# Kernel optimization log

Measured on AMD Instinct MI355X. Metric: run time of the kernel, lower is better.

Reference implementation:

```python
import jax, jax.numpy as jnp
import numpy as np

DIM = 1024
HEADS = 16
DIM_HEAD = 64
INNER = HEADS * DIM_HEAD
SCALE = DIM_HEAD ** -0.5
CAUSAL = True


def setup_inputs() -> dict:
    key = jax.random.key(0)
    k1, k2, k3, k4 = jax.random.split(key, 4)
    b, n = 4, 2048
    x = jax.random.normal(k1, (b, n, DIM), dtype=jnp.float32)
    mask = jnp.ones((b, n), dtype=bool)
    w_qkv = jax.random.normal(k2, (DIM, 3 * INNER), dtype=jnp.float32) * (DIM ** -0.5)
    w_out = jax.random.normal(k3, (INNER, DIM), dtype=jnp.float32) * (INNER ** -0.5)
    ln_g = jnp.ones((DIM,), dtype=jnp.float32)
    return {"x": x, "mask": mask, "w_qkv": w_qkv, "w_out": w_out, "ln_g": ln_g}


def clip_layernorm(x, g):
    eps = 1e-5 if x.dtype == jnp.float32 else 1e-3
    mean = jnp.mean(x, axis=-1, keepdims=True)
    var = jnp.var(x, axis=-1, keepdims=True)  # unbiased=False
    return (x - mean) * jax.lax.rsqrt(var + eps) * g


def reference(x, mask, w_qkv, w_out, ln_g):
    b, n, _ = x.shape
    qkv = x @ w_qkv  # [b, n, 3*inner]
    q, k, v = jnp.split(qkv, 3, axis=-1)
    split_heads = lambda t: t.reshape(b, n, HEADS, DIM_HEAD).transpose(0, 2, 1, 3)
    q, k, v = split_heads(q), split_heads(k), split_heads(v)
    q = q * SCALE
    sim = jnp.einsum('bhid,bhjd->bhij', q, k)
    mask_value = -jnp.finfo(sim.dtype).max
    sim = jnp.where(mask[:, None, None, :], sim, mask_value)
    if CAUSAL:
        causal_mask = jnp.triu(jnp.ones((n, n), dtype=bool), k=1)
        sim = jnp.where(causal_mask, mask_value, sim)
    attn = jax.nn.softmax(sim.astype(jnp.float32), axis=-1).astype(sim.dtype)
    out = jnp.einsum('bhij,bhjd->bhid', attn, v)
    out = out.transpose(0, 2, 1, 3).reshape(b, n, INNER)
    out = out @ w_out
    return clip_layernorm(out, ln_g)
```

## Files before the change

### kernel.cpp

```cpp
#include <hip/hip_runtime.h>


typedef unsigned short u16;
typedef __attribute__((ext_vector_type(8))) short bf16x8;
typedef __attribute__((ext_vector_type(4))) float f32x4;
typedef __attribute__((ext_vector_type(4))) unsigned short u16x4;
typedef __attribute__((ext_vector_type(2))) unsigned u32x2;

#define B_SZ  4
#define NSEQ  2048
#define DIMM  1024
#define NQKV  3072
#define MROWS 8192

#define AS_GLOBAL __attribute__((address_space(1)))
#define AS_LDS    __attribute__((address_space(3)))

__device__ __forceinline__ void async_copy16(void* lds, const void* g) {
  __builtin_amdgcn_global_load_lds((const AS_GLOBAL void*)g, (AS_LDS void*)lds, 16, 0, 0);
}

__device__ __forceinline__ u16 f32_to_bf16(float f) {
  unsigned u = __float_as_uint(f);
  u += 0x7FFFu + ((u >> 16) & 1u);
  return (u16)(u >> 16);
}

__device__ __forceinline__ unsigned cvt_pk_bf16(float a, float b) {
  unsigned r;
  asm("v_cvt_pk_bf16_f32 %0, %1, %2" : "=v"(r) : "v"(a), "v"(b));
  return r;
}


__global__ __launch_bounds__(256) void cvt_bf16_k(const float* __restrict__ in,
                                                  u16* __restrict__ out, int n4) {
  int i = blockIdx.x * 256 + threadIdx.x;
  if (i >= n4) return;
  f32x4 v = ((const f32x4*)in)[i];
  u16x4 o;
  #pragma unroll
  for (int c = 0; c < 4; ++c) o[c] = f32_to_bf16(v[c]);
  ((u16x4*)out)[i] = o;
}

__global__ __launch_bounds__(256) void tconv_k(const float* __restrict__ in,
                                               u16* __restrict__ out, int K, int N) {
  __shared__ float tile[64][65];
  int n0 = blockIdx.x * 64, k0 = blockIdx.y * 64;
  int t = threadIdx.x, tr = t >> 6, tc = t & 63;
  #pragma unroll
  for (int i = 0; i < 16; ++i)
    tile[tr + i * 4][tc] = in[(size_t)(k0 + tr + i * 4) * N + n0 + tc];
  __syncthreads();
  #pragma unroll
  for (int i = 0; i < 16; ++i)
    out[(size_t)(n0 + tr + i * 4) * K + k0 + tc] = f32_to_bf16(tile[tc][tr + i * 4]);
}


template<int WN>
__device__ __forceinline__ void gemm_mainloop(const u16* __restrict__ A, const u16* __restrict__ Bt,
                                              int K, size_t arow0, size_t brow0,
                                              u16* lA, u16* lB, f32x4 acc[8][4]) {
  constexpr int NW   = 2 * WN;
  constexpr int BN   = WN * 64;
  constexpr int ASZ  = 256 * 64;
  constexpr int BSZ  = BN * 64;
  constexpr int AIPW = 32 / NW;
  constexpr int BIPW = (BN / 8) / NW;
  const int t = threadIdx.x;
  const int w = t >> 6, lane = t & 63;
  const int l4 = lane >> 4, l15 = lane & 15;
  const int wrow = w / WN, wcol = w % WN;
  const int lr = lane >> 3, lc = lane & 7;

  auto stage = [&](int kt, int bufi) {
    u16* dA = lA + bufi * ASZ;
    u16* dB = lB + bufi * BSZ;
    #pragma unroll
    for (int j = 0; j < AIPW; ++j) {
      int r = w * (256 / NW) + j * 8 + lr;
      async_copy16(&dA[(size_t)r * 64 + lc * 8],
                   &A[(arow0 + r) * (size_t)K + kt + (lc ^ lr) * 8]);
    }
    #pragma unroll
    for (int j = 0; j < BIPW; ++j) {
      int r = w * (BN / NW) + j * 8 + lr;
      async_copy16(&dB[(size_t)r * 64 + lc * 8],
                   &Bt[(brow0 + r) * (size_t)K + kt + (lc ^ lr) * 8]);
    }
  };

  auto phase = [&](int bufi, int ch, bool do_stage, int kt_next, int bufn, bool gate) {
    const u16* bA = lA + bufi * ASZ;
    const u16* bB = lB + bufi * BSZ;
    bf16x8 af[8], bf[4];
    #pragma unroll
    for (int m = 0; m < 8; ++m) {
      int row = wrow * 128 + m * 16 + l15;
      af[m] = *(const bf16x8*)&bA[(size_t)row * 64 + ((ch * 4 + l4) ^ (row & 7)) * 8];
    }
    #pragma unroll
    for (int n = 0; n < 4; ++n) {
      int row = wcol * 64 + n * 16 + l15;
      bf[n] = *(const bf16x8*)&bB[(size_t)row * 64 + ((ch * 4 + l4) ^ (row & 7)) * 8];
    }
    if (do_stage) stage(kt_next, bufn);
    __builtin_amdgcn_s_barrier();
    asm volatile("s_waitcnt lgkmcnt(0)" ::: "memory");
    __builtin_amdgcn_sched_barrier(0);
    __builtin_amdgcn_s_setprio(1);
    #pragma unroll
    for (int m = 0; m < 8; ++m)
      #pragma unroll
      for (int n = 0; n < 4; ++n)
        acc[m][n] = __builtin_amdgcn_mfma_f32_16x16x32_bf16(af[m], bf[n], acc[m][n], 0, 0, 0);
    __builtin_amdgcn_s_setprio(0);
    if (gate) asm volatile("s_waitcnt vmcnt(0)" ::: "memory");
    __builtin_amdgcn_s_barrier();
  };

  const int T = K >> 6;
  stage(0, 0);
  asm volatile("s_waitcnt vmcnt(0)" ::: "memory");
  __builtin_amdgcn_s_barrier();
  #pragma unroll 1
  for (int s = 0; s < T; ++s) {
    const bool st = (s + 1 < T);
    phase(s & 1, 0, st, (s + 1) * 64, (s + 1) & 1, false);
    phase(s & 1, 1, false, 0, 0, st);
  }
}

__global__ __launch_bounds__(512, 2) void gemm_qkv_k(const u16* __restrict__ A, const u16* __restrict__ Bt,
                                                     u16* __restrict__ qb, u16* __restrict__ kb,
                                                     u16* __restrict__ vtb) {
  __shared__ u16 lA[2 * 256 * 64];
  __shared__ u16 lB[2 * 256 * 64];
  f32x4 acc[8][4];
  #pragma unroll
  for (int m = 0; m < 8; ++m)
    #pragma unroll
    for (int n = 0; n < 4; ++n) acc[m][n] = (f32x4){0.f, 0.f, 0.f, 0.f};
  gemm_mainloop<4>(A, Bt, DIMM, (size_t)blockIdx.y * 256, (size_t)blockIdx.x * 256, lA, lB, acc);
  const int t = threadIdx.x, w = t >> 6, lane = t & 63;
  const int l4 = lane >> 4, l15 = lane & 15;
  const int wrow = w >> 2, wcol = w & 3;
  const float QSCALE = 0.125f * 1.44269504089f;
  #pragma unroll
  for (int m = 0; m < 8; ++m)
    #pragma unroll
    for (int n = 0; n < 4; ++n)
      #pragma unroll
      for (int r = 0; r < 4; ++r) {
        int row = blockIdx.y * 256 + wrow * 128 + m * 16 + l4 * 4 + r;
        int col = blockIdx.x * 256 + wcol * 64 + n * 16 + l15;
        float v = acc[m][n][r];
        int bb = row >> 11, nr = row & 2047;
        int part = col >> 10, rem = col & 1023;
        int h = rem >> 6, d = rem & 63;
        int bh = bb * 16 + h;
        if (part == 0)      qb[((size_t)bh * NSEQ + nr) * 64 + d] = f32_to_bf16(v * QSCALE);
        else if (part == 1) kb[((size_t)bh * NSEQ + nr) * 64 + d] = f32_to_bf16(v);
        else                vtb[((size_t)bh * 64 + d) * NSEQ + nr] = f32_to_bf16(v);
      }
}

__global__ __launch_bounds__(256, 1) void gemm_out_k(const u16* __restrict__ A, const u16* __restrict__ Bt,
                                                     float* __restrict__ C) {
  __shared__ u16 lA[2 * 256 * 64];
  __shared__ u16 lB[2 * 128 * 64];
  f32x4 acc[8][4];
  #pragma unroll
  for (int m = 0; m < 8; ++m)
    #pragma unroll
    for (int n = 0; n < 4; ++n) acc[m][n] = (f32x4){0.f, 0.f, 0.f, 0.f};
  gemm_mainloop<2>(A, Bt, DIMM, (size_t)blockIdx.y * 256, (size_t)blockIdx.x * 128, lA, lB, acc);
  const int t = threadIdx.x, w = t >> 6, lane = t & 63;
  const int l4 = lane >> 4, l15 = lane & 15;
  const int wrow = w >> 1, wcol = w & 1;
  #pragma unroll
  for (int m = 0; m < 8; ++m)
    #pragma unroll
    for (int n = 0; n < 4; ++n)
      #pragma unroll
      for (int r = 0; r < 4; ++r) {
        int row = blockIdx.y * 256 + wrow * 128 + m * 16 + l4 * 4 + r;
        int col = blockIdx.x * 128 + wcol * 64 + n * 16 + l15;
        C[(size_t)row * DIMM + col] = acc[m][n][r];
      }
}


__global__ __launch_bounds__(512, 4) void attn_k(const u16* __restrict__ qb, const u16* __restrict__ kb,
                                                 const u16* __restrict__ vtb, u16* __restrict__ ao) {
  __shared__ u16 lK[2][64 * 64];
  __shared__ u16 lV[2][64 * 64];
  __shared__ u16 lP[8][16 * 64];
  const int bh = blockIdx.y;
  const int t = threadIdx.x, w = t >> 6, l = t & 63;
  const int l4 = l >> 4, l15 = l & 15;
  const int b = bh >> 4, h = bh & 15;
  u16* lPw = lP[w];

  const int srow = t >> 3;
  const int ssc = (t & 7) ^ (srow & 7);

  #pragma unroll 1
  for (int phase = 0; phase < 2; ++phase) {
    const int qt = phase == 0 ? (int)blockIdx.x : 15 - (int)blockIdx.x;
    const int q0w = qt * 128 + w * 16;

    bf16x8 qf0 = *(const bf16x8*)&qb[((size_t)bh * NSEQ + q0w + l15) * 64 + l4 * 8];
    bf16x8 qf1 = *(const bf16x8*)&qb[((size_t)bh * NSEQ + q0w + l15) * 64 + 32 + l4 * 8];

    float m_r = -1e30f, l_r = 0.f;
    f32x4 o[4];
    #pragma unroll
    for (int d = 0; d < 4; ++d) o[d] = (f32x4){0.f, 0.f, 0.f, 0.f};

    const int njt = 2 * qt + 2;

    {
      async_copy16(&lK[0][t * 8], &kb[((size_t)bh * NSEQ + srow) * 64 + ssc * 8]);
      async_copy16(&lV[0][t * 8], &vtb[((size_t)bh * 64 + srow) * NSEQ + ssc * 8]);
    }
    int buf = 0;

    for (int jt = 0; jt < njt; ++jt) {
      __syncthreads();
      if (jt + 1 < njt) {
        int bsel = buf ^ 1, jn = jt + 1;
        async_copy16(&lK[bsel][t * 8], &kb[((size_t)bh * NSEQ + jn * 64 + srow) * 64 + ssc * 8]);
        async_copy16(&lV[bsel][t * 8], &vtb[((size_t)bh * 64 + srow) * NSEQ + (size_t)jn * 64 + ssc * 8]);
      }
      const int jt64 = jt * 64;
      if (jt64 > q0w + 15) { buf ^= 1; continue; }
      const u16* Kb = lK[buf];
      const u16* Vb = lV[buf];

      bf16x8 kf[4][2];
      #pragma unroll
      for (int nf = 0; nf < 4; ++nf)
        #pragma unroll
        for (int kk = 0; kk < 2; ++kk)
          kf[nf][kk] = *(const bf16x8*)&Kb[(nf * 16 + l15) * 64 + ((kk * 4 + l4) ^ (l15 & 7)) * 8];

      f32x4 z[4];
      __builtin_amdgcn_s_setprio(1);
      #pragma unroll
      for (int nf = 0; nf < 4; ++nf) {
        f32x4 zz = (f32x4){0.f, 0.f, 0.f, 0.f};
        zz = __builtin_amdgcn_mfma_f32_16x16x32_bf16(kf[nf][0], qf0, zz, 0, 0, 0);
        zz = __builtin_amdgcn_mfma_f32_16x16x32_bf16(kf[nf][1], qf1, zz, 0, 0, 0);
        z[nf] = zz;
      }
      __builtin_amdgcn_s_setprio(0);

      bf16x8 bv[4][2];
      #pragma unroll
      for (int dd = 0; dd < 4; ++dd)
        #pragma unroll
        for (int kk = 0; kk < 2; ++kk)
          bv[dd][kk] = *(const bf16x8*)&Vb[(dd * 16 + l15) * 64 + ((kk * 4 + l4) ^ (l15 & 7)) * 8];

      if (jt64 + 63 > q0w) {
        #pragma unroll
        for (int nf = 0; nf < 4; ++nf)
          #pragma unroll
          for (int r = 0; r < 4; ++r)
            if (jt64 + nf * 16 + l4 * 4 + r > q0w + l15) z[nf][r] = -1e30f;
      }

      float mt = fmaxf(fmaxf(z[0][0], z[0][1]), fmaxf(z[0][2], z[0][3]));
      #pragma unroll
      for (int nf = 1; nf < 4; ++nf)
        mt = fmaxf(mt, fmaxf(fmaxf(z[nf][0], z[nf][1]), fmaxf(z[nf][2], z[nf][3])));
      mt = fmaxf(mt, __shfl_xor(mt, 16));
      mt = fmaxf(mt, __shfl_xor(mt, 32));

      if (!__all(mt <= m_r + 8.f)) {
        float nm = fmaxf(m_r, mt);
        float sc = __builtin_amdgcn_exp2f(m_r - nm);
        m_r = nm;
        l_r *= sc;
        float scr[4];
        #pragma unroll
        for (int r = 0; r < 4; ++r) scr[r] = __shfl(sc, l4 * 4 + r);
        #pragma unroll
        for (int d = 0; d < 4; ++d)
          #pragma unroll
          for (int r = 0; r < 4; ++r) o[d][r] *= scr[r];
      }

      float rs = 0.f;
      unsigned pk[4][2];
      #pragma unroll
      for (int nf = 0; nf < 4; ++nf)
        #pragma unroll
        for (int hh = 0; hh < 2; ++hh) {
          float p0 = __builtin_amdgcn_exp2f(z[nf][2 * hh]     - m_r);
          float p1 = __builtin_amdgcn_exp2f(z[nf][2 * hh + 1] - m_r);
          rs += p0 + p1;
          pk[nf][hh] = cvt_pk_bf16(p0, p1);
        }
      rs += __shfl_xor(rs, 16);
      rs += __shfl_xor(rs, 32);
      l_r += rs;

      #pragma unroll
      for (int nf = 0; nf < 4; ++nf) {
        int u = (2 * nf + (l4 >> 1)) ^ (l15 & 7);
        *(u32x2*)&lPw[l15 * 64 + u * 8 + (l4 & 1) * 4] = (u32x2){pk[nf][0], pk[nf][1]};
      }
      __builtin_amdgcn_sched_barrier(0);
      int u0 = l4 ^ (l15 & 7), u1 = (4 + l4) ^ (l15 & 7);
      bf16x8 af0 = *(const bf16x8*)&lPw[l15 * 64 + u0 * 8];
      bf16x8 af1 = *(const bf16x8*)&lPw[l15 * 64 + u1 * 8];

      __builtin_amdgcn_s_setprio(1);
      #pragma unroll
      for (int d = 0; d < 4; ++d) {
        o[d] = __builtin_amdgcn_mfma_f32_16x16x32_bf16(af0, bv[d][0], o[d], 0, 0, 0);
        o[d] = __builtin_amdgcn_mfma_f32_16x16x32_bf16(af1, bv[d][1], o[d], 0, 0, 0);
      }
      __builtin_amdgcn_s_setprio(0);
      buf ^= 1;
    }

    float lv[4];
    #pragma unroll
    for (int r = 0; r < 4; ++r) lv[r] = __shfl(l_r, l4 * 4 + r);
    #pragma unroll
    for (int d = 0; d < 4; ++d)
      #pragma unroll
      for (int r = 0; r < 4; ++r) {
        int nrow = q0w + l4 * 4 + r;
        float vv = o[d][r] / lv[r];
        ao[((size_t)(b * NSEQ + nrow)) * 1024 + h * 64 + d * 16 + l15] = f32_to_bf16(vv);
      }
  }
}

__global__ __launch_bounds__(256) void ln_k(float* __restrict__ io, const float* __restrict__ g) {
  const int row = blockIdx.x, t = threadIdx.x;
  const int w = t >> 6, l = t & 63;
  f32x4 v = ((const f32x4*)(io + (size_t)row * DIMM))[t];
  float s = v[0] + v[1] + v[2] + v[3];
  float q = v[0] * v[0] + v[1] * v[1] + v[2] * v[2] + v[3] * v[3];
  #pragma unroll
  for (int off = 1; off < 64; off <<= 1) { s += __shfl_xor(s, off); q += __shfl_xor(q, off); }
  __shared__ float ss[8];
  if (l == 0) { ss[w] = s; ss[4 + w] = q; }
  __syncthreads();
  s = ss[0] + ss[1] + ss[2] + ss[3];
  q = ss[4] + ss[5] + ss[6] + ss[7];
  float mean = s * (1.f / DIMM);
  float var = q * (1.f / DIMM) - mean * mean;
  float rstd = rsqrtf(var + 1e-5f);
  f32x4 gv = ((const f32x4*)g)[t];
  f32x4 y;
  #pragma unroll
  for (int c = 0; c < 4; ++c) y[c] = (v[c] - mean) * rstd * gv[c];
  ((f32x4*)(io + (size_t)row * DIMM))[t] = y;
}

extern "C" void kernel_launch(void* const* d_in, const int* in_sizes, int n_in,
                              void* d_out, int out_size, void* d_ws, size_t ws_size,
                              hipStream_t stream) {
  const float* x     = (const float*)d_in[0];
  const float* w_qkv = (const float*)d_in[2];
  const float* w_out = (const float*)d_in[3];
  const float* ln_g  = (const float*)d_in[4];
  float* out = (float*)d_out;

  char* ws = (char*)d_ws;
  const size_t MB = 1u << 20;
  u16* x_bf   = (u16*)(ws);
  u16* wqkv_t = (u16*)(ws + 16 * MB);
  u16* wout_t = (u16*)(ws + 22 * MB);
  u16* qb     = (u16*)(ws + 24 * MB);
  u16* kb     = (u16*)(ws + 40 * MB);
  u16* vtb    = (u16*)(ws + 56 * MB);
  u16* attn_o = x_bf;

  cvt_bf16_k<<<8192, 256, 0, stream>>>(x, x_bf, (MROWS * DIMM) / 4);
  tconv_k<<<dim3(NQKV / 64, DIMM / 64), 256, 0, stream>>>(w_qkv, wqkv_t, DIMM, NQKV);
  tconv_k<<<dim3(DIMM / 64, DIMM / 64), 256, 0, stream>>>(w_out, wout_t, DIMM, DIMM);
  gemm_qkv_k<<<dim3(NQKV / 256, MROWS / 256), 512, 0, stream>>>(x_bf, wqkv_t, qb, kb, vtb);
  attn_k<<<dim3(8, B_SZ * 16), 512, 0, stream>>>(qb, kb, vtb, attn_o);
  gemm_out_k<<<dim3(DIMM / 128, MROWS / 256), 256, 0, stream>>>(attn_o, wout_t, out);
  ln_k<<<MROWS, 256, 0, stream>>>(out, ln_g);
}
```

Baseline: 227.2 us.

## Restructure GEMM mainloop into four-phase split staging and shrink out-proj tiles

Replaces the two-phase GEMM mainloop with a four-quadrant schedule. A and B tiles are staged in halves interleaved between MFMA groups, and partial vmcnt waits let global-to-LDS copies overlap compute at finer granularity. The output projection GEMM moves from 256x128 to 128x128 tiles with two blocks per CU, doubling the grid for better occupancy and load balance. The risk is extra barrier and LDS-read overhead, plus the correctness of the partial vmcnt accounting.

```diff
diff --git a/kernel.cpp b/kernel.cpp
--- a/kernel.cpp
+++ b/kernel.cpp
@@ -59,77 +59,126 @@
 }
 
 
-template<int WN>
-__device__ __forceinline__ void gemm_mainloop(const u16* __restrict__ A, const u16* __restrict__ Bt,
-                                              int K, size_t arow0, size_t brow0,
-                                              u16* lA, u16* lB, f32x4 acc[8][4]) {
-  constexpr int NW   = 2 * WN;
-  constexpr int BN   = WN * 64;
-  constexpr int ASZ  = 256 * 64;
-  constexpr int BSZ  = BN * 64;
-  constexpr int AIPW = 32 / NW;
-  constexpr int BIPW = (BN / 8) / NW;
+template<int BM, int BN, int NW, int MR>
+__device__ __forceinline__ void gemm_loop(const u16* __restrict__ A, const u16* __restrict__ Bt,
+                                          int K, size_t arow0, size_t brow0,
+                                          u16* lA, u16* lB, f32x4 (&acc)[MR][4]) {
+  constexpr int WN  = BN / 64;
+  constexpr int MH  = MR / 2;
+  constexpr int WTM = 16 * MR;
+  constexpr int ASZ = BM * 64;
+  constexpr int BSZ = BN * 64;
   const int t = threadIdx.x;
   const int w = t >> 6, lane = t & 63;
   const int l4 = lane >> 4, l15 = lane & 15;
   const int wrow = w / WN, wcol = w % WN;
   const int lr = lane >> 3, lc = lane & 7;
 
-  auto stage = [&](int kt, int bufi) {
-    u16* dA = lA + bufi * ASZ;
-    u16* dB = lB + bufi * BSZ;
-    #pragma unroll
-    for (int j = 0; j < AIPW; ++j) {
-      int r = w * (256 / NW) + j * 8 + lr;
-      async_copy16(&dA[(size_t)r * 64 + lc * 8],
-                   &A[(arow0 + r) * (size_t)K + kt + (lc ^ lr) * 8]);
-    }
-    #pragma unroll
-    for (int j = 0; j < BIPW; ++j) {
-      int r = w * (BN / NW) + j * 8 + lr;
-      async_copy16(&dB[(size_t)r * 64 + lc * 8],
-                   &Bt[(brow0 + r) * (size_t)K + kt + (lc ^ lr) * 8]);
+  auto stageA = [&](int kt, int bufi, int h) {
+    u16* d = lA + bufi * ASZ;
+    #pragma unroll
+    for (int j = 0; j < BM / (16 * NW); ++j) {
+      int rr = w * (BM / (2 * NW)) + j * 8 + lr;
+      int r  = (h + 2 * (rr / (WTM / 2))) * (WTM / 2) + (rr % (WTM / 2));
+      async_copy16(&d[(size_t)r * 64 + lc * 8],
+                   &A[(arow0 + r) * (size_t)K + kt + (lc ^ (r & 7)) * 8]);
     }
   };
-
-  auto phase = [&](int bufi, int ch, bool do_stage, int kt_next, int bufn, bool gate) {
-    const u16* bA = lA + bufi * ASZ;
-    const u16* bB = lB + bufi * BSZ;
-    bf16x8 af[8], bf[4];
-    #pragma unroll
-    for (int m = 0; m < 8; ++m) {
-      int row = wrow * 128 + m * 16 + l15;
-      af[m] = *(const bf16x8*)&bA[(size_t)row * 64 + ((ch * 4 + l4) ^ (row & 7)) * 8];
+  auto stageB = [&](int kt, int bufi, int h) {
+    u16* d = lB + bufi * BSZ;
+    #pragma unroll
+    for (int j = 0; j < BN / (16 * NW); ++j) {
+      int r = h * (BN / 2) + w * (BN / (2 * NW)) + j * 8 + lr;
+      async_copy16(&d[(size_t)r * 64 + lc * 8],
+                   &Bt[(brow0 + r) * (size_t)K + kt + (lc ^ (r & 7)) * 8]);
+    }
+  };
+
+  const int T = K >> 6;
+  stageA(0, 0, 0); stageB(0, 0, 0); stageB(0, 0, 1); stageA(0, 0, 1);
+
+  #pragma unroll 1
+  for (int s = 0; s < T; ++s) {
+    const u16* bA = lA + (s & 1) * ASZ;
+    const u16* bB = lB + (s & 1) * BSZ;
+    const bool st = (s + 1 < T);
+    const int kn = (s + 1) * 64, bn = (s + 1) & 1;
+    bf16x8 af[MH], bf0[4], bf1[4];
+
+    asm volatile("s_waitcnt vmcnt(2)" ::: "memory");
+    __builtin_amdgcn_s_barrier();
+    __builtin_amdgcn_sched_barrier(0);
+    #pragma unroll
+    for (int m = 0; m < MH; ++m) {
+      int row = wrow * WTM + m * 16 + l15;
+      af[m] = *(const bf16x8*)&bA[(size_t)row * 64 + ((l4) ^ (row & 7)) * 8];
     }
     #pragma unroll
     for (int n = 0; n < 4; ++n) {
       int row = wcol * 64 + n * 16 + l15;
-      bf[n] = *(const bf16x8*)&bB[(size_t)row * 64 + ((ch * 4 + l4) ^ (row & 7)) * 8];
-    }
-    if (do_stage) stage(kt_next, bufn);
+      bf0[n] = *(const bf16x8*)&bB[(size_t)row * 64 + ((l4) ^ (row & 7)) * 8];
+      bf1[n] = *(const bf16x8*)&bB[(size_t)row * 64 + ((4 + l4) ^ (row & 7)) * 8];
+    }
+    if (st) stageA(kn, bn, 0);
+    asm volatile("s_waitcnt lgkmcnt(0)" ::: "memory");
+    __builtin_amdgcn_sched_barrier(0);
+    __builtin_amdgcn_s_setprio(1);
+    #pragma unroll
+    for (int m = 0; m < MH; ++m)
+      #pragma unroll
+      for (int n = 0; n < 4; ++n)
+        acc[m][n] = __builtin_amdgcn_mfma_f32_16x16x32_bf16(af[m], bf0[n], acc[m][n], 0, 0, 0);
+    __builtin_amdgcn_s_setprio(0);
+    #pragma unroll
+    for (int m = 0; m < MH; ++m) {
+      int row = wrow * WTM + m * 16 + l15;
+      af[m] = *(const bf16x8*)&bA[(size_t)row * 64 + ((4 + l4) ^ (row & 7)) * 8];
+    }
+    if (st) stageB(kn, bn, 0);
+    asm volatile("s_waitcnt lgkmcnt(0)" ::: "memory");
+    __builtin_amdgcn_sched_barrier(0);
+    __builtin_amdgcn_s_setprio(1);
+    #pragma unroll
+    for (int m = 0; m < MH; ++m)
+      #pragma unroll
+      for (int n = 0; n < 4; ++n)
+        acc[m][n] = __builtin_amdgcn_mfma_f32_16x16x32_bf16(af[m], bf1[n], acc[m][n], 0, 0, 0);
+    __builtin_amdgcn_s_setprio(0);
+
+    if (st) asm volatile("s_waitcnt vmcnt(4)" ::: "memory");
+    else    asm volatile("s_waitcnt vmcnt(0)" ::: "memory");
     __builtin_amdgcn_s_barrier();
+    __builtin_amdgcn_sched_barrier(0);
+    #pragma unroll
+    for (int m = 0; m < MH; ++m) {
+      int row = wrow * WTM + (MH + m) * 16 + l15;
+      af[m] = *(const bf16x8*)&bA[(size_t)row * 64 + ((l4) ^ (row & 7)) * 8];
+    }
+    if (st) stageB(kn, bn, 1);
     asm volatile("s_waitcnt lgkmcnt(0)" ::: "memory");
     __builtin_amdgcn_sched_barrier(0);
     __builtin_amdgcn_s_setprio(1);
     #pragma unroll
-    for (int m = 0; m < 8; ++m)
+    for (int m = 0; m < MH; ++m)
       #pragma unroll
       for (int n = 0; n < 4; ++n)
-        acc[m][n] = __builtin_amdgcn_mfma_f32_16x16x32_bf16(af[m], bf[n], acc[m][n], 0, 0, 0);
+        acc[MH + m][n] = __builtin_amdgcn_mfma_f32_16x16x32_bf16(af[m], bf0[n], acc[MH + m][n], 0, 0, 0);
     __builtin_amdgcn_s_setprio(0);
-    if (gate) asm volatile("s_waitcnt vmcnt(0)" ::: "memory");
-    __builtin_amdgcn_s_barrier();
-  };
-
-  const int T = K >> 6;
-  stage(0, 0);
-  asm volatile("s_waitcnt vmcnt(0)" ::: "memory");
-  __builtin_amdgcn_s_barrier();
-  #pragma unroll 1
-  for (int s = 0; s < T; ++s) {
-    const bool st = (s + 1 < T);
-    phase(s & 1, 0, st, (s + 1) * 64, (s + 1) & 1, false);
-    phase(s & 1, 1, false, 0, 0, st);
+    #pragma unroll
+    for (int m = 0; m < MH; ++m) {
+      int row = wrow * WTM + (MH + m) * 16 + l15;
+      af[m] = *(const bf16x8*)&bA[(size_t)row * 64 + ((4 + l4) ^ (row & 7)) * 8];
+    }
+    if (st) stageA(kn, bn, 1);
+    asm volatile("s_waitcnt lgkmcnt(0)" ::: "memory");
+    __builtin_amdgcn_sched_barrier(0);
+    __builtin_amdgcn_s_setprio(1);
+    #pragma unroll
+    for (int m = 0; m < MH; ++m)
+      #pragma unroll
+      for (int n = 0; n < 4; ++n)
+        acc[MH + m][n] = __builtin_amdgcn_mfma_f32_16x16x32_bf16(af[m], bf1[n], acc[MH + m][n], 0, 0, 0);
+    __builtin_amdgcn_s_setprio(0);
   }
 }
 
@@ -143,7 +192,7 @@
   for (int m = 0; m < 8; ++m)
     #pragma unroll
     for (int n = 0; n < 4; ++n) acc[m][n] = (f32x4){0.f, 0.f, 0.f, 0.f};
-  gemm_mainloop<4>(A, Bt, DIMM, (size_t)blockIdx.y * 256, (size_t)blockIdx.x * 256, lA, lB, acc);
+  gemm_loop<256, 256, 8, 8>(A, Bt, DIMM, (size_t)blockIdx.y * 256, (size_t)blockIdx.x * 256, lA, lB, acc);
   const int t = threadIdx.x, w = t >> 6, lane = t & 63;
   const int l4 = lane >> 4, l15 = lane & 15;
   const int wrow = w >> 2, wcol = w & 3;
@@ -167,26 +216,26 @@
       }
 }
 
-__global__ __launch_bounds__(256, 1) void gemm_out_k(const u16* __restrict__ A, const u16* __restrict__ Bt,
+__global__ __launch_bounds__(256, 2) void gemm_out_k(const u16* __restrict__ A, const u16* __restrict__ Bt,
                                                      float* __restrict__ C) {
-  __shared__ u16 lA[2 * 256 * 64];
+  __shared__ u16 lA[2 * 128 * 64];
   __shared__ u16 lB[2 * 128 * 64];
-  f32x4 acc[8][4];
-  #pragma unroll
-  for (int m = 0; m < 8; ++m)
+  f32x4 acc[4][4];
+  #pragma unroll
+  for (int m = 0; m < 4; ++m)
     #pragma unroll
     for (int n = 0; n < 4; ++n) acc[m][n] = (f32x4){0.f, 0.f, 0.f, 0.f};
-  gemm_mainloop<2>(A, Bt, DIMM, (size_t)blockIdx.y * 256, (size_t)blockIdx.x * 128, lA, lB, acc);
+  gemm_loop<128, 128, 4, 4>(A, Bt, DIMM, (size_t)blockIdx.y * 128, (size_t)blockIdx.x * 128, lA, lB, acc);
   const int t = threadIdx.x, w = t >> 6, lane = t & 63;
   const int l4 = lane >> 4, l15 = lane & 15;
   const int wrow = w >> 1, wcol = w & 1;
   #pragma unroll
-  for (int m = 0; m < 8; ++m)
+  for (int m = 0; m < 4; ++m)
     #pragma unroll
     for (int n = 0; n < 4; ++n)
       #pragma unroll
       for (int r = 0; r < 4; ++r) {
-        int row = blockIdx.y * 256 + wrow * 128 + m * 16 + l4 * 4 + r;
+        int row = blockIdx.y * 128 + wrow * 64 + m * 16 + l4 * 4 + r;
         int col = blockIdx.x * 128 + wcol * 64 + n * 16 + l15;
         C[(size_t)row * DIMM + col] = acc[m][n][r];
       }
@@ -390,6 +439,6 @@
   tconv_k<<<dim3(DIMM / 64, DIMM / 64), 256, 0, stream>>>(w_out, wout_t, DIMM, DIMM);
   gemm_qkv_k<<<dim3(NQKV / 256, MROWS / 256), 512, 0, stream>>>(x_bf, wqkv_t, qb, kb, vtb);
   attn_k<<<dim3(8, B_SZ * 16), 512, 0, stream>>>(qb, kb, vtb, attn_o);
-  gemm_out_k<<<dim3(DIMM / 128, MROWS / 256), 256, 0, stream>>>(attn_o, wout_t, out);
+  gemm_out_k<<<dim3(DIMM / 128, MROWS / 128), 256, 0, stream>>>(attn_o, wout_t, out);
   ln_k<<<MROWS, 256, 0, stream>>>(out, ln_g);
 }
```

Measured after the change: 210.1 us. 1.08x faster.
